# Kernel optimization log

Measured on AMD Instinct MI355X. Metric: run time of the kernel, lower is better.

Reference implementation:

```python
import jax, jax.numpy as jnp
import numpy as np

ETA = 0.01
EPSILON = 1e-08


def setup_inputs() -> dict:
    key = jax.random.key(0)
    k1, k2 = jax.random.split(key)
    B, N = 2000000, 16  # batch (time steps), num_assets
    weights = jax.random.uniform(k1, (B, N), dtype=jnp.float32)
    next_returns = jax.random.normal(k2, (B, N), dtype=jnp.float32) * 0.02
    return {"weights": weights, "next_returns": next_returns}


def reference(weights, next_returns):
    # portfolio return per time step: (B,)
    R = jnp.sum(weights * next_returns, axis=1)
    batch_size = R.shape[0]
    eta = jnp.asarray(ETA, R.dtype)
    eps = jnp.asarray(EPSILON, R.dtype)

    def step(carry, R_t):
        A_prev, B_prev = carry
        delta_A = eta * (R_t - A_prev)
        delta_B = eta * (R_t * R_t - B_prev)
        variance = jnp.maximum(B_prev - A_prev * A_prev, eps)
        denom = variance ** 1.5
        D_t = (B_prev * delta_A - 0.5 * A_prev * delta_B) / denom
        return (A_prev + delta_A, B_prev + delta_B), D_t

    init = (jnp.asarray(0.0, R.dtype), jnp.asarray(EPSILON, R.dtype))
    _, D = jax.lax.scan(step, init, R)
    return -jnp.sum(D) / batch_size
```

## Files before the change

kernel.cpp:

```cpp
#include <hip/hip_runtime.h>


#define D_ETA 0.01
#define D_C   (1.0 - D_ETA)
#define D_EPS 1e-8

constexpr int BLOCK = 256;
constexpr int CHUNK = 2048;
constexpr int LPT   = CHUNK / BLOCK;
__device__ __forceinline__ int pidx(int i) { return i + (i >> 3); }
constexpr int RS_SIZE = CHUNK + CHUNK / 8;

__device__ __forceinline__ double row_R(const float* __restrict__ w,
                                        const float* __restrict__ x,
                                        long long row) {
    const float4* w4 = (const float4*)(w + row * 16);
    const float4* x4 = (const float4*)(x + row * 16);
    double r = 0.0;
#pragma unroll
    for (int q = 0; q < 4; ++q) {
        float4 a = w4[q];
        float4 b = x4[q];
        r += (double)a.x * (double)b.x;
        r += (double)a.y * (double)b.y;
        r += (double)a.z * (double)b.z;
        r += (double)a.w * (double)b.w;
    }
    return r;
}

__device__ __forceinline__ void block_scan(double& m, double& sA, double& sB,
                                           double* mS, double* aS, double* bS) {
    int tid = threadIdx.x;
    mS[tid] = m; aS[tid] = sA; bS[tid] = sB;
    __syncthreads();
#pragma unroll
    for (int off = 1; off < BLOCK; off <<= 1) {
        double pm = 1.0, pa = 0.0, pb = 0.0;
        if (tid >= off) { pm = mS[tid - off]; pa = aS[tid - off]; pb = bS[tid - off]; }
        __syncthreads();
        if (tid >= off) {
            sA = m * pa + sA;
            sB = m * pb + sB;
            m  = pm * m;
        }
        mS[tid] = m; aS[tid] = sA; bS[tid] = sB;
        __syncthreads();
    }
}

__global__ __launch_bounds__(BLOCK) void k1_partials(
    const float* __restrict__ w, const float* __restrict__ x, int nrows,
    float* __restrict__ Rws,
    double* __restrict__ blkM, double* __restrict__ blkA, double* __restrict__ blkB)
{
    __shared__ float Rs[RS_SIZE];
    __shared__ double mS[BLOCK], aS[BLOCK], bS[BLOCK];
    int tid = threadIdx.x;
    long long base = (long long)blockIdx.x * CHUNK;

#pragma unroll
    for (int j = 0; j < LPT; ++j) {
        int idx = j * BLOCK + tid;
        long long row = base + idx;
        float rv = 0.f;
        if (row < nrows) {
            rv = (float)row_R(w, x, row);
            if (Rws) Rws[row] = rv;
        }
        Rs[pidx(idx)] = rv;
    }
    __syncthreads();

    int start = tid * LPT;
    long long grow = base + start;
    long long rem = (long long)nrows - grow;
    int len = rem >= LPT ? LPT : (rem > 0 ? (int)rem : 0);

    double m = 1.0, sA = 0.0, sB = 0.0;
    for (int k = 0; k < len; ++k) {
        double r = (double)Rs[pidx(start + k)];
        sA = D_C * sA + D_ETA * r;
        sB = D_C * sB + D_ETA * (r * r);
        m *= D_C;
    }
    block_scan(m, sA, sB, mS, aS, bS);
    if (tid == BLOCK - 1) {
        blkM[blockIdx.x] = m;
        blkA[blockIdx.x] = sA;
        blkB[blockIdx.x] = sB;
    }
}

__global__ __launch_bounds__(BLOCK) void k2_scan(
    int nb,
    const double* __restrict__ blkM, const double* __restrict__ blkA,
    const double* __restrict__ blkB,
    double* __restrict__ A0, double* __restrict__ B0)
{
    __shared__ double mS[BLOCK], aS[BLOCK], bS[BLOCK];
    int tid = threadIdx.x;
    int K = (nb + BLOCK - 1) / BLOCK;
    int g0 = tid * K;
    int g1 = g0 + K; if (g1 > nb) g1 = nb;

    double m = 1.0, sA = 0.0, sB = 0.0;
    for (int g = g0; g < g1; ++g) {
        double mg = blkM[g], ag = blkA[g], bg = blkB[g];
        sA = mg * sA + ag;
        sB = mg * sB + bg;
        m *= mg;
    }
    block_scan(m, sA, sB, mS, aS, bS);

    double em = 1.0, ea = 0.0, eb = 0.0;
    if (tid > 0) { em = mS[tid - 1]; ea = aS[tid - 1]; eb = bS[tid - 1]; }
    double A = ea;
    double B = em * D_EPS + eb;
    for (int g = g0; g < g1; ++g) {
        A0[g] = A; B0[g] = B;
        double mg = blkM[g], ag = blkA[g], bg = blkB[g];
        A = mg * A + ag;
        B = mg * B + bg;
    }
}

__global__ __launch_bounds__(BLOCK) void k3_dsum(
    const float* __restrict__ w, const float* __restrict__ x, int nrows,
    const float* __restrict__ Rws,
    const double* __restrict__ A0, const double* __restrict__ B0,
    double* __restrict__ bsum)
{
    __shared__ float Rs[RS_SIZE];
    __shared__ double mS[BLOCK], aS[BLOCK], bS[BLOCK];
    __shared__ double wsum[BLOCK / 64];
    int tid = threadIdx.x;
    long long base = (long long)blockIdx.x * CHUNK;

#pragma unroll
    for (int j = 0; j < LPT; ++j) {
        int idx = j * BLOCK + tid;
        long long row = base + idx;
        float rv = 0.f;
        if (row < nrows) {
            if (Rws) rv = Rws[row];
            else     rv = (float)row_R(w, x, row);
        }
        Rs[pidx(idx)] = rv;
    }
    __syncthreads();

    int start = tid * LPT;
    long long grow = base + start;
    long long rem = (long long)nrows - grow;
    int len = rem >= LPT ? LPT : (rem > 0 ? (int)rem : 0);

    double m = 1.0, sA = 0.0, sB = 0.0;
    for (int k = 0; k < len; ++k) {
        double r = (double)Rs[pidx(start + k)];
        sA = D_C * sA + D_ETA * r;
        sB = D_C * sB + D_ETA * (r * r);
        m *= D_C;
    }
    block_scan(m, sA, sB, mS, aS, bS);

    double em = 1.0, ea = 0.0, eb = 0.0;
    if (tid > 0) { em = mS[tid - 1]; ea = aS[tid - 1]; eb = bS[tid - 1]; }
    double A = em * A0[blockIdx.x] + ea;
    double B = em * B0[blockIdx.x] + eb;

    double dsum = 0.0;
    for (int k = 0; k < len; ++k) {
        double r = (double)Rs[pidx(start + k)];
        double dA = D_ETA * (r - A);
        double dB = D_ETA * (r * r - B);
        double var = B - A * A;
        if (var < D_EPS) var = D_EPS;
        double denom = var * sqrt(var);
        dsum += (B * dA - 0.5 * A * dB) / denom;
        A += dA;
        B += dB;
    }

#pragma unroll
    for (int off = 32; off > 0; off >>= 1) dsum += __shfl_down(dsum, off, 64);
    if ((tid & 63) == 0) wsum[tid >> 6] = dsum;
    __syncthreads();
    if (tid == 0) {
        double s = wsum[0] + wsum[1] + wsum[2] + wsum[3];
        bsum[blockIdx.x] = s;
    }
}

__global__ __launch_bounds__(BLOCK) void k4_final(
    const double* __restrict__ bsum, int nb, int nrows, float* __restrict__ out)
{
    __shared__ double sh[BLOCK / 64];
    int tid = threadIdx.x;
    double s = 0.0;
    for (int i = tid; i < nb; i += BLOCK) s += bsum[i];
#pragma unroll
    for (int off = 32; off > 0; off >>= 1) s += __shfl_down(s, off, 64);
    if ((tid & 63) == 0) sh[tid >> 6] = s;
    __syncthreads();
    if (tid == 0) {
        double t = sh[0] + sh[1] + sh[2] + sh[3];
        out[0] = (float)(-t / (double)nrows);
    }
}

extern "C" void kernel_launch(void* const* d_in, const int* in_sizes, int n_in,
                              void* d_out, int out_size, void* d_ws, size_t ws_size,
                              hipStream_t stream)
{
    const float* w = (const float*)d_in[0];
    const float* x = (const float*)d_in[1];
    int nrows = in_sizes[0] / 16;
    int nb = (nrows + CHUNK - 1) / CHUNK;

    char* ws = (char*)d_ws;
    double* blkM = (double*)(ws + 64);
    double* blkA = blkM + nb;
    double* blkB = blkA + nb;
    double* A0   = blkB + nb;
    double* B0   = A0 + nb;
    double* bsum = B0 + nb;
    size_t off = 64 + (size_t)6 * nb * sizeof(double);
    off = (off + 255) & ~(size_t)255;
    float* Rws = nullptr;
    if (ws_size >= off + (size_t)nrows * sizeof(float))
        Rws = (float*)(ws + off);

    k1_partials<<<nb, BLOCK, 0, stream>>>(w, x, nrows, Rws, blkM, blkA, blkB);
    k2_scan<<<1, BLOCK, 0, stream>>>(nb, blkM, blkA, blkB, A0, B0);
    k3_dsum<<<nb, BLOCK, 0, stream>>>(w, x, nrows, Rws, A0, B0, bsum);
    k4_final<<<1, BLOCK, 0, stream>>>(bsum, nb, nrows, (float*)d_out);
}
```

Baseline: 287.8 us.

## Split dot products into coalesced kernel and load scan segments into registers

Adds a separate kernel that computes the per-row dot products with four threads per row, using float4 loads that are coalesced across the wavefront and a shuffle reduction. The result is written to a workspace buffer. The partials and dsum kernels then read each thread's eight contiguous R values directly into registers with float4 loads, replacing the shared-memory staging buffer. This removes the strided per-row loads and the LDS round trip. The cost is one extra kernel launch and an extra write and read pass over the R array.

```diff
diff --git a/kernel.cpp b/kernel.cpp
--- a/kernel.cpp
+++ b/kernel.cpp
@@ -6,14 +6,13 @@
 #define D_EPS 1e-8
 
 constexpr int BLOCK = 256;
+constexpr int K1_ROWS = 256;
 constexpr int CHUNK = 2048;
 constexpr int LPT   = CHUNK / BLOCK;
-__device__ __forceinline__ int pidx(int i) { return i + (i >> 3); }
-constexpr int RS_SIZE = CHUNK + CHUNK / 8;
-
-__device__ __forceinline__ double row_R(const float* __restrict__ w,
-                                        const float* __restrict__ x,
-                                        long long row) {
+
+__device__ __forceinline__ float row_R(const float* __restrict__ w,
+                                       const float* __restrict__ x,
+                                       long long row) {
     const float4* w4 = (const float4*)(w + row * 16);
     const float4* x4 = (const float4*)(x + row * 16);
     double r = 0.0;
@@ -26,7 +25,35 @@
         r += (double)a.z * (double)b.z;
         r += (double)a.w * (double)b.w;
     }
-    return r;
+    return (float)r;
+}
+
+__global__ __launch_bounds__(BLOCK) void k1_dots(
+    const float* __restrict__ w, const float* __restrict__ x, int nrows,
+    float* __restrict__ R)
+{
+    int tid = threadIdx.x;
+    int q    = tid & 3;
+    int rsub = tid >> 2;
+    long long base = (long long)blockIdx.x * K1_ROWS;
+    const float4* w4 = (const float4*)w;
+    const float4* x4 = (const float4*)x;
+#pragma unroll
+    for (int it = 0; it < K1_ROWS / 64; ++it) {
+        long long row = base + (long long)it * 64 + rsub;
+        if (row < nrows) {
+            long long f = row * 4 + q;
+            float4 a = w4[f];
+            float4 b = x4[f];
+            double p = (double)a.x * (double)b.x
+                     + (double)a.y * (double)b.y
+                     + (double)a.z * (double)b.z
+                     + (double)a.w * (double)b.w;
+            p += __shfl_xor(p, 1, 64);
+            p += __shfl_xor(p, 2, 64);
+            if (q == 0) R[row] = (float)p;
+        }
+    }
 }
 
 __device__ __forceinline__ void block_scan(double& m, double& sA, double& sB,
@@ -49,37 +76,41 @@
     }
 }
 
-__global__ __launch_bounds__(BLOCK) void k1_partials(
+__device__ __forceinline__ int load_seg(const float* __restrict__ Rws,
+                                        const float* __restrict__ w,
+                                        const float* __restrict__ x,
+                                        long long g0, int nrows, float* rv) {
+    long long rem = (long long)nrows - g0;
+    int len = rem >= LPT ? LPT : (rem > 0 ? (int)rem : 0);
+    if (Rws) {
+        if (len == LPT) {
+            const float4* Rp = (const float4*)(Rws + g0);
+            float4 u = Rp[0], v = Rp[1];
+            rv[0]=u.x; rv[1]=u.y; rv[2]=u.z; rv[3]=u.w;
+            rv[4]=v.x; rv[5]=v.y; rv[6]=v.z; rv[7]=v.w;
+        } else {
+            for (int k = 0; k < len; ++k) rv[k] = Rws[g0 + k];
+        }
+    } else {
+        for (int k = 0; k < len; ++k) rv[k] = row_R(w, x, g0 + k);
+    }
+    return len;
+}
+
+__global__ __launch_bounds__(BLOCK) void k2_partials(
+    const float* __restrict__ Rws,
     const float* __restrict__ w, const float* __restrict__ x, int nrows,
-    float* __restrict__ Rws,
     double* __restrict__ blkM, double* __restrict__ blkA, double* __restrict__ blkB)
 {
-    __shared__ float Rs[RS_SIZE];
     __shared__ double mS[BLOCK], aS[BLOCK], bS[BLOCK];
     int tid = threadIdx.x;
-    long long base = (long long)blockIdx.x * CHUNK;
-
-#pragma unroll
-    for (int j = 0; j < LPT; ++j) {
-        int idx = j * BLOCK + tid;
-        long long row = base + idx;
-        float rv = 0.f;
-        if (row < nrows) {
-            rv = (float)row_R(w, x, row);
-            if (Rws) Rws[row] = rv;
-        }
-        Rs[pidx(idx)] = rv;
-    }
-    __syncthreads();
-
-    int start = tid * LPT;
-    long long grow = base + start;
-    long long rem = (long long)nrows - grow;
-    int len = rem >= LPT ? LPT : (rem > 0 ? (int)rem : 0);
+    long long g0 = (long long)blockIdx.x * CHUNK + (long long)tid * LPT;
+    float rv[LPT];
+    int len = load_seg(Rws, w, x, g0, nrows, rv);
 
     double m = 1.0, sA = 0.0, sB = 0.0;
     for (int k = 0; k < len; ++k) {
-        double r = (double)Rs[pidx(start + k)];
+        double r = (double)rv[k];
         sA = D_C * sA + D_ETA * r;
         sB = D_C * sB + D_ETA * (r * r);
         m *= D_C;
@@ -92,7 +123,7 @@
     }
 }
 
-__global__ __launch_bounds__(BLOCK) void k2_scan(
+__global__ __launch_bounds__(BLOCK) void k3_scan(
     int nb,
     const double* __restrict__ blkM, const double* __restrict__ blkA,
     const double* __restrict__ blkB,
@@ -125,39 +156,22 @@
     }
 }
 
-__global__ __launch_bounds__(BLOCK) void k3_dsum(
+__global__ __launch_bounds__(BLOCK) void k4_dsum(
+    const float* __restrict__ Rws,
     const float* __restrict__ w, const float* __restrict__ x, int nrows,
-    const float* __restrict__ Rws,
     const double* __restrict__ A0, const double* __restrict__ B0,
     double* __restrict__ bsum)
 {
-    __shared__ float Rs[RS_SIZE];
     __shared__ double mS[BLOCK], aS[BLOCK], bS[BLOCK];
     __shared__ double wsum[BLOCK / 64];
     int tid = threadIdx.x;
-    long long base = (long long)blockIdx.x * CHUNK;
-
-#pragma unroll
-    for (int j = 0; j < LPT; ++j) {
-        int idx = j * BLOCK + tid;
-        long long row = base + idx;
-        float rv = 0.f;
-        if (row < nrows) {
-            if (Rws) rv = Rws[row];
-            else     rv = (float)row_R(w, x, row);
-        }
-        Rs[pidx(idx)] = rv;
-    }
-    __syncthreads();
-
-    int start = tid * LPT;
-    long long grow = base + start;
-    long long rem = (long long)nrows - grow;
-    int len = rem >= LPT ? LPT : (rem > 0 ? (int)rem : 0);
+    long long g0 = (long long)blockIdx.x * CHUNK + (long long)tid * LPT;
+    float rv[LPT];
+    int len = load_seg(Rws, w, x, g0, nrows, rv);
 
     double m = 1.0, sA = 0.0, sB = 0.0;
     for (int k = 0; k < len; ++k) {
-        double r = (double)Rs[pidx(start + k)];
+        double r = (double)rv[k];
         sA = D_C * sA + D_ETA * r;
         sB = D_C * sB + D_ETA * (r * r);
         m *= D_C;
@@ -171,7 +185,7 @@
 
     double dsum = 0.0;
     for (int k = 0; k < len; ++k) {
-        double r = (double)Rs[pidx(start + k)];
+        double r = (double)rv[k];
         double dA = D_ETA * (r - A);
         double dB = D_ETA * (r * r - B);
         double var = B - A * A;
@@ -186,13 +200,10 @@
     for (int off = 32; off > 0; off >>= 1) dsum += __shfl_down(dsum, off, 64);
     if ((tid & 63) == 0) wsum[tid >> 6] = dsum;
     __syncthreads();
-    if (tid == 0) {
-        double s = wsum[0] + wsum[1] + wsum[2] + wsum[3];
-        bsum[blockIdx.x] = s;
-    }
-}
-
-__global__ __launch_bounds__(BLOCK) void k4_final(
+    if (tid == 0) bsum[blockIdx.x] = wsum[0] + wsum[1] + wsum[2] + wsum[3];
+}
+
+__global__ __launch_bounds__(BLOCK) void k5_final(
     const double* __restrict__ bsum, int nb, int nrows, float* __restrict__ out)
 {
     __shared__ double sh[BLOCK / 64];
@@ -203,10 +214,7 @@
     for (int off = 32; off > 0; off >>= 1) s += __shfl_down(s, off, 64);
     if ((tid & 63) == 0) sh[tid >> 6] = s;
     __syncthreads();
-    if (tid == 0) {
-        double t = sh[0] + sh[1] + sh[2] + sh[3];
-        out[0] = (float)(-t / (double)nrows);
-    }
+    if (tid == 0) out[0] = (float)(-(sh[0] + sh[1] + sh[2] + sh[3]) / (double)nrows);
 }
 
 extern "C" void kernel_launch(void* const* d_in, const int* in_sizes, int n_in,
@@ -216,7 +224,8 @@
     const float* w = (const float*)d_in[0];
     const float* x = (const float*)d_in[1];
     int nrows = in_sizes[0] / 16;
-    int nb = (nrows + CHUNK - 1) / CHUNK;
+    int nb  = (nrows + CHUNK - 1) / CHUNK;
+    int nb1 = (nrows + K1_ROWS - 1) / K1_ROWS;
 
     char* ws = (char*)d_ws;
     double* blkM = (double*)(ws + 64);
@@ -231,8 +240,10 @@
     if (ws_size >= off + (size_t)nrows * sizeof(float))
         Rws = (float*)(ws + off);
 
-    k1_partials<<<nb, BLOCK, 0, stream>>>(w, x, nrows, Rws, blkM, blkA, blkB);
-    k2_scan<<<1, BLOCK, 0, stream>>>(nb, blkM, blkA, blkB, A0, B0);
-    k3_dsum<<<nb, BLOCK, 0, stream>>>(w, x, nrows, Rws, A0, B0, bsum);
-    k4_final<<<1, BLOCK, 0, stream>>>(bsum, nb, nrows, (float*)d_out);
-}
+    if (Rws)
+        k1_dots<<<nb1, BLOCK, 0, stream>>>(w, x, nrows, Rws);
+    k2_partials<<<nb, BLOCK, 0, stream>>>(Rws, w, x, nrows, blkM, blkA, blkB);
+    k3_scan<<<1, BLOCK, 0, stream>>>(nb, blkM, blkA, blkB, A0, B0);
+    k4_dsum<<<nb, BLOCK, 0, stream>>>(Rws, w, x, nrows, A0, B0, bsum);
+    k5_final<<<1, BLOCK, 0, stream>>>(bsum, nb, nrows, (float*)d_out);
+}
```

After: 286.5 us (median of 2 runs). No clear change (-0.5%).

## Fuse scan pipeline into single-pass decoupled look-back kernel

Applied to the files above, without the earlier changes.

Replaces the four-kernel pipeline (partials, block-prefix scan, recompute D-sum, final reduce) with one persistent-ticket kernel. The kernel computes R once, publishes per-chunk aggregates, and resolves its exclusive prefix through decoupled look-back with flags. The final sum uses atomic accumulation and a last-block-done counter. Loads are also restructured so that four lanes share one row with coalesced float4 reads and shuffle reductions. This removes the second pass over the inputs, the intermediate R buffer and extra launches, at the cost of serial spin-waits on predecessor chunks and nondeterministic summation order.

```diff
diff --git a/kernel.cpp b/kernel.cpp
--- a/kernel.cpp
+++ b/kernel.cpp
@@ -8,25 +8,13 @@
 constexpr int BLOCK = 256;
 constexpr int CHUNK = 2048;
 constexpr int LPT   = CHUNK / BLOCK;
-__device__ __forceinline__ int pidx(int i) { return i + (i >> 3); }
-constexpr int RS_SIZE = CHUNK + CHUNK / 8;
-
-__device__ __forceinline__ double row_R(const float* __restrict__ w,
-                                        const float* __restrict__ x,
-                                        long long row) {
-    const float4* w4 = (const float4*)(w + row * 16);
-    const float4* x4 = (const float4*)(x + row * 16);
-    double r = 0.0;
-#pragma unroll
-    for (int q = 0; q < 4; ++q) {
-        float4 a = w4[q];
-        float4 b = x4[q];
-        r += (double)a.x * (double)b.x;
-        r += (double)a.y * (double)b.y;
-        r += (double)a.z * (double)b.z;
-        r += (double)a.w * (double)b.w;
-    }
-    return r;
+constexpr int GRP   = CHUNK / 64;
+
+#define SCOPE __HIP_MEMORY_SCOPE_AGENT
+
+__device__ __forceinline__ double dot4d(float4 a, float4 b) {
+    return (double)a.x * (double)b.x + (double)a.y * (double)b.y
+         + (double)a.z * (double)b.z + (double)a.w * (double)b.w;
 }
 
 __device__ __forceinline__ void block_scan(double& m, double& sA, double& sB,
@@ -49,129 +37,133 @@
     }
 }
 
-__global__ __launch_bounds__(BLOCK) void k1_partials(
-    const float* __restrict__ w, const float* __restrict__ x, int nrows,
-    float* __restrict__ Rws,
-    double* __restrict__ blkM, double* __restrict__ blkA, double* __restrict__ blkB)
+__global__ __launch_bounds__(BLOCK) void k0_init(unsigned* __restrict__ ctl,
+                                                 int nctl)
 {
-    __shared__ float Rs[RS_SIZE];
+    int i = blockIdx.x * BLOCK + threadIdx.x;
+    if (i < nctl) ctl[i] = 0u;
+}
+
+__global__ __launch_bounds__(BLOCK) void k_mega(
+    const float* __restrict__ w, const float* __restrict__ x,
+    int nrows, int nb,
+    unsigned* __restrict__ ticket,
+    unsigned* __restrict__ flags,
+    double*   __restrict__ recs,
+    double*   __restrict__ acc,
+    unsigned* __restrict__ done,
+    float*    __restrict__ out)
+{
+    __shared__ float  Rs[CHUNK];
     __shared__ double mS[BLOCK], aS[BLOCK], bS[BLOCK];
+    __shared__ double exA, exB;
+    __shared__ double wsum[BLOCK / 64];
+    __shared__ unsigned s_cid;
+
     int tid = threadIdx.x;
-    long long base = (long long)blockIdx.x * CHUNK;
-
+    if (tid == 0)
+        s_cid = __hip_atomic_fetch_add(ticket, 1u, __ATOMIC_RELAXED, SCOPE);
+    __syncthreads();
+    int cid = (int)s_cid;
+    long long base = (long long)cid * CHUNK;
+
+    int q    = tid & 3;
+    int rsub = tid >> 2;
+    const float4* w4 = (const float4*)w;
+    const float4* x4 = (const float4*)x;
+    long long f0 = base * 4 + tid;
+
+    if (base + CHUNK <= (long long)nrows) {
 #pragma unroll
-    for (int j = 0; j < LPT; ++j) {
-        int idx = j * BLOCK + tid;
-        long long row = base + idx;
-        float rv = 0.f;
-        if (row < nrows) {
-            rv = (float)row_R(w, x, row);
-            if (Rws) Rws[row] = rv;
-        }
-        Rs[pidx(idx)] = rv;
+        for (int g = 0; g < GRP; g += 4) {
+            float4 a0 = w4[f0 + (long long)(g + 0) * 256];
+            float4 a1 = w4[f0 + (long long)(g + 1) * 256];
+            float4 a2 = w4[f0 + (long long)(g + 2) * 256];
+            float4 a3 = w4[f0 + (long long)(g + 3) * 256];
+            float4 b0 = x4[f0 + (long long)(g + 0) * 256];
+            float4 b1 = x4[f0 + (long long)(g + 1) * 256];
+            float4 b2 = x4[f0 + (long long)(g + 2) * 256];
+            float4 b3 = x4[f0 + (long long)(g + 3) * 256];
+            double p0 = dot4d(a0, b0), p1 = dot4d(a1, b1);
+            double p2 = dot4d(a2, b2), p3 = dot4d(a3, b3);
+            p0 += __shfl_xor(p0, 1, 64); p0 += __shfl_xor(p0, 2, 64);
+            p1 += __shfl_xor(p1, 1, 64); p1 += __shfl_xor(p1, 2, 64);
+            p2 += __shfl_xor(p2, 1, 64); p2 += __shfl_xor(p2, 2, 64);
+            p3 += __shfl_xor(p3, 1, 64); p3 += __shfl_xor(p3, 2, 64);
+            if (q == 0) {
+                Rs[(g + 0) * 64 + rsub] = (float)p0;
+                Rs[(g + 1) * 64 + rsub] = (float)p1;
+                Rs[(g + 2) * 64 + rsub] = (float)p2;
+                Rs[(g + 3) * 64 + rsub] = (float)p3;
+            }
+        }
+    } else {
+        for (int g = 0; g < GRP; ++g) {
+            long long row = base + g * 64 + rsub;
+            double p = 0.0;
+            if (row < nrows) {
+                float4 a = w4[row * 4 + q];
+                float4 b = x4[row * 4 + q];
+                p = dot4d(a, b);
+            }
+            p += __shfl_xor(p, 1, 64);
+            p += __shfl_xor(p, 2, 64);
+            if (q == 0) Rs[g * 64 + rsub] = (float)p;
+        }
     }
     __syncthreads();
 
     int start = tid * LPT;
-    long long grow = base + start;
-    long long rem = (long long)nrows - grow;
+    long long rem = (long long)nrows - (base + start);
     int len = rem >= LPT ? LPT : (rem > 0 ? (int)rem : 0);
 
     double m = 1.0, sA = 0.0, sB = 0.0;
     for (int k = 0; k < len; ++k) {
-        double r = (double)Rs[pidx(start + k)];
+        double r = (double)Rs[start + k];
         sA = D_C * sA + D_ETA * r;
         sB = D_C * sB + D_ETA * (r * r);
         m *= D_C;
     }
     block_scan(m, sA, sB, mS, aS, bS);
+
     if (tid == BLOCK - 1) {
-        blkM[blockIdx.x] = m;
-        blkA[blockIdx.x] = sA;
-        blkB[blockIdx.x] = sB;
-    }
-}
-
-__global__ __launch_bounds__(BLOCK) void k2_scan(
-    int nb,
-    const double* __restrict__ blkM, const double* __restrict__ blkA,
-    const double* __restrict__ blkB,
-    double* __restrict__ A0, double* __restrict__ B0)
-{
-    __shared__ double mS[BLOCK], aS[BLOCK], bS[BLOCK];
-    int tid = threadIdx.x;
-    int K = (nb + BLOCK - 1) / BLOCK;
-    int g0 = tid * K;
-    int g1 = g0 + K; if (g1 > nb) g1 = nb;
-
-    double m = 1.0, sA = 0.0, sB = 0.0;
-    for (int g = g0; g < g1; ++g) {
-        double mg = blkM[g], ag = blkA[g], bg = blkB[g];
-        sA = mg * sA + ag;
-        sB = mg * sB + bg;
-        m *= mg;
-    }
-    block_scan(m, sA, sB, mS, aS, bS);
+        double* rc = recs + (size_t)cid * 6;
+        __hip_atomic_store(&rc[0], m,  __ATOMIC_RELAXED, SCOPE);
+        __hip_atomic_store(&rc[1], sA, __ATOMIC_RELAXED, SCOPE);
+        __hip_atomic_store(&rc[2], sB, __ATOMIC_RELAXED, SCOPE);
+        __hip_atomic_store(&flags[cid], 1u, __ATOMIC_RELEASE, SCOPE);
+
+        double cm = 1.0, ca = 0.0, cb = 0.0;
+        for (int j = cid - 1; j >= 0; --j) {
+            unsigned f;
+            while ((f = __hip_atomic_load(&flags[j], __ATOMIC_ACQUIRE, SCOPE)) == 0u)
+                __builtin_amdgcn_s_sleep(2);
+            const double* rj = recs + (size_t)j * 6 + (f == 2u ? 3 : 0);
+            double jm = __hip_atomic_load(&rj[0], __ATOMIC_RELAXED, SCOPE);
+            double ja = __hip_atomic_load(&rj[1], __ATOMIC_RELAXED, SCOPE);
+            double jb = __hip_atomic_load(&rj[2], __ATOMIC_RELAXED, SCOPE);
+            ca = cm * ja + ca;
+            cb = cm * jb + cb;
+            cm = cm * jm;
+            if (f == 2u) break;
+        }
+        __hip_atomic_store(&rc[3], m * cm,       __ATOMIC_RELAXED, SCOPE);
+        __hip_atomic_store(&rc[4], m * ca + sA,  __ATOMIC_RELAXED, SCOPE);
+        __hip_atomic_store(&rc[5], m * cb + sB,  __ATOMIC_RELAXED, SCOPE);
+        __hip_atomic_store(&flags[cid], 2u, __ATOMIC_RELEASE, SCOPE);
+        exA = ca;
+        exB = cm * D_EPS + cb;
+    }
+    __syncthreads();
 
     double em = 1.0, ea = 0.0, eb = 0.0;
     if (tid > 0) { em = mS[tid - 1]; ea = aS[tid - 1]; eb = bS[tid - 1]; }
-    double A = ea;
-    double B = em * D_EPS + eb;
-    for (int g = g0; g < g1; ++g) {
-        A0[g] = A; B0[g] = B;
-        double mg = blkM[g], ag = blkA[g], bg = blkB[g];
-        A = mg * A + ag;
-        B = mg * B + bg;
-    }
-}
-
-__global__ __launch_bounds__(BLOCK) void k3_dsum(
-    const float* __restrict__ w, const float* __restrict__ x, int nrows,
-    const float* __restrict__ Rws,
-    const double* __restrict__ A0, const double* __restrict__ B0,
-    double* __restrict__ bsum)
-{
-    __shared__ float Rs[RS_SIZE];
-    __shared__ double mS[BLOCK], aS[BLOCK], bS[BLOCK];
-    __shared__ double wsum[BLOCK / 64];
-    int tid = threadIdx.x;
-    long long base = (long long)blockIdx.x * CHUNK;
-
-#pragma unroll
-    for (int j = 0; j < LPT; ++j) {
-        int idx = j * BLOCK + tid;
-        long long row = base + idx;
-        float rv = 0.f;
-        if (row < nrows) {
-            if (Rws) rv = Rws[row];
-            else     rv = (float)row_R(w, x, row);
-        }
-        Rs[pidx(idx)] = rv;
-    }
-    __syncthreads();
-
-    int start = tid * LPT;
-    long long grow = base + start;
-    long long rem = (long long)nrows - grow;
-    int len = rem >= LPT ? LPT : (rem > 0 ? (int)rem : 0);
-
-    double m = 1.0, sA = 0.0, sB = 0.0;
-    for (int k = 0; k < len; ++k) {
-        double r = (double)Rs[pidx(start + k)];
-        sA = D_C * sA + D_ETA * r;
-        sB = D_C * sB + D_ETA * (r * r);
-        m *= D_C;
-    }
-    block_scan(m, sA, sB, mS, aS, bS);
-
-    double em = 1.0, ea = 0.0, eb = 0.0;
-    if (tid > 0) { em = mS[tid - 1]; ea = aS[tid - 1]; eb = bS[tid - 1]; }
-    double A = em * A0[blockIdx.x] + ea;
-    double B = em * B0[blockIdx.x] + eb;
+    double A = em * exA + ea;
+    double B = em * exB + eb;
 
     double dsum = 0.0;
     for (int k = 0; k < len; ++k) {
-        double r = (double)Rs[pidx(start + k)];
+        double r = (double)Rs[start + k];
         double dA = D_ETA * (r - A);
         double dB = D_ETA * (r * r - B);
         double var = B - A * A;
@@ -186,26 +178,15 @@
     for (int off = 32; off > 0; off >>= 1) dsum += __shfl_down(dsum, off, 64);
     if ((tid & 63) == 0) wsum[tid >> 6] = dsum;
     __syncthreads();
+
     if (tid == 0) {
-        double s = wsum[0] + wsum[1] + wsum[2] + wsum[3];
-        bsum[blockIdx.x] = s;
-    }
-}
-
-__global__ __launch_bounds__(BLOCK) void k4_final(
-    const double* __restrict__ bsum, int nb, int nrows, float* __restrict__ out)
-{
-    __shared__ double sh[BLOCK / 64];
-    int tid = threadIdx.x;
-    double s = 0.0;
-    for (int i = tid; i < nb; i += BLOCK) s += bsum[i];
-#pragma unroll
-    for (int off = 32; off > 0; off >>= 1) s += __shfl_down(s, off, 64);
-    if ((tid & 63) == 0) sh[tid >> 6] = s;
-    __syncthreads();
-    if (tid == 0) {
-        double t = sh[0] + sh[1] + sh[2] + sh[3];
-        out[0] = (float)(-t / (double)nrows);
+        double bs = wsum[0] + wsum[1] + wsum[2] + wsum[3];
+        __hip_atomic_fetch_add(acc, bs, __ATOMIC_RELAXED, SCOPE);
+        unsigned r = __hip_atomic_fetch_add(done, 1u, __ATOMIC_ACQ_REL, SCOPE);
+        if (r == (unsigned)(nb - 1)) {
+            double total = __hip_atomic_load(acc, __ATOMIC_RELAXED, SCOPE);
+            out[0] = (float)(-total / (double)nrows);
+        }
     }
 }
 
@@ -218,21 +199,16 @@
     int nrows = in_sizes[0] / 16;
     int nb = (nrows + CHUNK - 1) / CHUNK;
 
-    char* ws = (char*)d_ws;
-    double* blkM = (double*)(ws + 64);
-    double* blkA = blkM + nb;
-    double* blkB = blkA + nb;
-    double* A0   = blkB + nb;
-    double* B0   = A0 + nb;
-    double* bsum = B0 + nb;
-    size_t off = 64 + (size_t)6 * nb * sizeof(double);
-    off = (off + 255) & ~(size_t)255;
-    float* Rws = nullptr;
-    if (ws_size >= off + (size_t)nrows * sizeof(float))
-        Rws = (float*)(ws + off);
-
-    k1_partials<<<nb, BLOCK, 0, stream>>>(w, x, nrows, Rws, blkM, blkA, blkB);
-    k2_scan<<<1, BLOCK, 0, stream>>>(nb, blkM, blkA, blkB, A0, B0);
-    k3_dsum<<<nb, BLOCK, 0, stream>>>(w, x, nrows, Rws, A0, B0, bsum);
-    k4_final<<<1, BLOCK, 0, stream>>>(bsum, nb, nrows, (float*)d_out);
-}
+    unsigned* ctl    = (unsigned*)d_ws;
+    unsigned* ticket = ctl + 0;
+    unsigned* done   = ctl + 1;
+    double*   acc    = (double*)(ctl + 2);
+    unsigned* flags  = ctl + 4;
+    int nctl = 4 + nb;
+    size_t recs_off = ((size_t)nctl * 4 + 255) & ~(size_t)255;
+    double* recs = (double*)((char*)d_ws + recs_off);
+
+    k0_init<<<(nctl + BLOCK - 1) / BLOCK, BLOCK, 0, stream>>>(ctl, nctl);
+    k_mega<<<nb, BLOCK, 0, stream>>>(w, x, nrows, nb, ticket, flags, recs,
+                                     acc, done, (float*)d_out);
+}
```

Result: slower. 599.9 us (+108.5%).
